# Kernel tuning notes

Hardware: AMD Instinct MI355X
Metric: run time of the kernel (lower is better)

## Reference

```python
import jax, jax.numpy as jnp
import numpy as np

B, N, D, E = 2, 50000, 128, 500000
LN_EPS = 1e-5


def setup_inputs() -> dict:
    key = jax.random.key(0)
    k_h, k_e, k_ws, k_wm = jax.random.split(key, 4)
    scale = 1.0 / np.sqrt(D).astype(np.float32)
    return {
        "h": jax.random.normal(k_h, (B, N, D), dtype=jnp.float32),
        "edge_index": jax.random.randint(k_e, (2, E), 0, N, dtype=jnp.int64),
        "W_self": jax.random.normal(k_ws, (D, D), dtype=jnp.float32) * scale,
        "W_msg": jax.random.normal(k_wm, (D, D), dtype=jnp.float32) * scale,
        "bias": jnp.zeros((D,), dtype=jnp.float32),
        "gamma": jnp.ones((D,), dtype=jnp.float32),
        "beta": jnp.zeros((D,), dtype=jnp.float32),
    }


def reference(h, edge_index, W_self, W_msg, bias, gamma, beta):
    # h: [B,N,D]; edge_index: [2,E] with rows (src, dst).
    n = h.shape[1]
    src, dst = edge_index[0], edge_index[1]

    # Self transform: Linear(dim, dim, bias=False) -> h @ W_self.T
    h_self = jnp.einsum("bnd,od->bno", h, W_self)

    # Gather src node features and transform: msg = W_msg(h[:, src, :])
    msg = jnp.einsum("bed,od->beo", h[:, src, :], W_msg)  # [B,E,D]

    # Scatter-add mean aggregation onto dst nodes.
    h_agg = jax.vmap(lambda m: jax.ops.segment_sum(m, dst, num_segments=n))(msg)  # [B,N,D]
    count = jax.ops.segment_sum(jnp.ones((dst.shape[0],), h.dtype), dst, num_segments=n)
    count = jnp.clip(count, 1.0)[None, :, None]  # clamp(min=1)
    h_agg = h_agg / count

    # Residual + ReLU + (dropout in eval = identity) + LayerNorm
    x = h + jax.nn.relu(h_self + h_agg + bias)
    mu = jnp.mean(x, axis=-1, keepdims=True)
    var = jnp.mean(jnp.square(x - mu), axis=-1, keepdims=True)
    return (x - mu) * jax.lax.rsqrt(var + LN_EPS) * gamma + beta
```

## Files before the change

### kernel.cpp

```cpp
#include <hip/hip_runtime.h>

#define NB 2
#define NN 50000
#define ND 128
#define NE 500000
#define NM (NB * NN)
#define LN_EPS 1e-5f

typedef __attribute__((ext_vector_type(8))) short short8;
typedef __attribute__((ext_vector_type(4))) float f32x4;
typedef __attribute__((ext_vector_type(4))) unsigned short us4;

#define HB_OFF     0
#define AGG_OFF    25600000
#define DEG_OFF    51200000
#define START_OFF  51400000
#define CURSOR_OFF 51600192
#define ELIST_OFF  51800192
#define PART_OFF   53800192
#define WMSG_OFF   53801216

#define SCAN_BLK 512
#define SCAN_NB ((NN + SCAN_BLK - 1) / SCAN_BLK)

__device__ __forceinline__ unsigned short f32_to_bf16(float f) {
    unsigned u = __builtin_bit_cast(unsigned, f);
    unsigned r = u + 0x7FFFu + ((u >> 16) & 1u);
    return (unsigned short)(r >> 16);
}

__device__ __forceinline__ float bf16_to_f32(unsigned short s) {
    unsigned u = ((unsigned)s) << 16;
    return __builtin_bit_cast(float, u);
}

__global__ void count_kernel(const int* __restrict__ ei, int* __restrict__ deg) {
    int e = blockIdx.x * blockDim.x + threadIdx.x;
    if (e < NE) {
        atomicAdd(&deg[ei[NE + e]], 1);
    }
}

__global__ void block_reduce_kernel(const int* __restrict__ deg, int* __restrict__ partials) {
    int i = blockIdx.x * SCAN_BLK + threadIdx.x;
    int v = (i < NN) ? deg[i] : 0;
#pragma unroll
    for (int off = 32; off > 0; off >>= 1) v += __shfl_down(v, off);
    __shared__ int wsum[SCAN_BLK / 64];
    int lane = threadIdx.x & 63;
    int w = threadIdx.x >> 6;
    if (lane == 0) wsum[w] = v;
    __syncthreads();
    if (threadIdx.x == 0) {
        int s = 0;
#pragma unroll
        for (int k = 0; k < SCAN_BLK / 64; ++k) s += wsum[k];
        partials[blockIdx.x] = s;
    }
}

__global__ void partial_scan_kernel(int* __restrict__ partials) {
    __shared__ int tmp[128];
    int t = threadIdx.x;
    int v = (t < SCAN_NB) ? partials[t] : 0;
    tmp[t] = v;
    __syncthreads();
    for (int off = 1; off < 128; off <<= 1) {
        int u = (t >= off) ? tmp[t - off] : 0;
        __syncthreads();
        tmp[t] += u;
        __syncthreads();
    }
    if (t < SCAN_NB) partials[t] = tmp[t] - v;
}

__global__ void block_scan_kernel(const int* __restrict__ deg, const int* __restrict__ partials,
                                  int* __restrict__ start, int* __restrict__ cursor) {
    __shared__ int tmp[SCAN_BLK];
    int t = threadIdx.x;
    int i = blockIdx.x * SCAN_BLK + t;
    int v = (i < NN) ? deg[i] : 0;
    tmp[t] = v;
    __syncthreads();
    for (int off = 1; off < SCAN_BLK; off <<= 1) {
        int u = (t >= off) ? tmp[t - off] : 0;
        __syncthreads();
        tmp[t] += u;
        __syncthreads();
    }
    if (i < NN) {
        int excl = tmp[t] - v + partials[blockIdx.x];
        start[i] = excl;
        cursor[i] = excl;
    }
    if (i == 0) start[NN] = NE;
}

__global__ void fill_kernel(const int* __restrict__ ei, int* __restrict__ cursor,
                            int* __restrict__ elist) {
    int e = blockIdx.x * blockDim.x + threadIdx.x;
    if (e < NE) {
        int d = ei[NE + e];
        int p = atomicAdd(&cursor[d], 1);
        elist[p] = ei[e];
    }
}

__global__ void convert_h_kernel(const float* __restrict__ h, unsigned short* __restrict__ hb16) {
    int i = blockIdx.x * blockDim.x + threadIdx.x;
    if (i >= NM * 16) return;
    int row = i >> 4;
    int c = i & 15;
    const float4 v0 = *(const float4*)(h + (size_t)row * ND + c * 8);
    const float4 v1 = *(const float4*)(h + (size_t)row * ND + c * 8 + 4);
    short8 o;
    o[0] = (short)f32_to_bf16(v0.x); o[1] = (short)f32_to_bf16(v0.y);
    o[2] = (short)f32_to_bf16(v0.z); o[3] = (short)f32_to_bf16(v0.w);
    o[4] = (short)f32_to_bf16(v1.x); o[5] = (short)f32_to_bf16(v1.y);
    o[6] = (short)f32_to_bf16(v1.z); o[7] = (short)f32_to_bf16(v1.w);
    *(short8*)(hb16 + (size_t)row * ND + c * 8) = o;
}

__global__ void convert_wmsg_kernel(const float* __restrict__ Wmsg, unsigned short* __restrict__ wmsg16) {
    int i = blockIdx.x * blockDim.x + threadIdx.x;
    if (i >= 128 * 16) return;
    int row = i >> 4;
    int c = i & 15;
    const float* src = Wmsg + (size_t)row * ND + c * 8;
    short8 o;
#pragma unroll
    for (int j = 0; j < 8; ++j) o[j] = (short)f32_to_bf16(src[j]);
    *(short8*)(wmsg16 + (size_t)row * ND + c * 8) = o;
}

__global__ void agg_kernel(const unsigned short* __restrict__ hb16, const int* __restrict__ start,
                           const int* __restrict__ elist, unsigned short* __restrict__ agg) {
    int wid = (blockIdx.x * blockDim.x + threadIdx.x) >> 6;
    int l = threadIdx.x & 63;
    if (wid >= NM) return;
    int b = wid / NN;
    int n = wid - b * NN;
    int s0 = start[n];
    int d = start[n + 1] - s0;
    const int g = l >> 4;
    const int li = l & 15;
    const unsigned short* hb = hb16 + (size_t)b * NN * ND;
    float s[8] = {0.f, 0.f, 0.f, 0.f, 0.f, 0.f, 0.f, 0.f};
    for (int j0 = 0; j0 < d; j0 += 64) {
        int mye = (j0 + l < d) ? elist[s0 + j0 + l] : -1;
        int cnt = (d - j0 < 64) ? (d - j0) : 64;
        for (int p = 0; p < cnt; p += 4) {
            int e = __shfl(mye, p + g);
            if (p + g < cnt) {
                const short8 v = *(const short8*)(hb + (size_t)e * ND + li * 8);
#pragma unroll
                for (int j = 0; j < 8; ++j) s[j] += bf16_to_f32((unsigned short)v[j]);
            }
        }
    }
#pragma unroll
    for (int j = 0; j < 8; ++j) {
        s[j] += __shfl_xor(s[j], 16);
        s[j] += __shfl_xor(s[j], 32);
    }
    if (g == 0) {
        float sc = 1.0f / (float)(d > 1 ? d : 1);
        short8 o;
#pragma unroll
        for (int j = 0; j < 8; ++j) o[j] = (short)f32_to_bf16(s[j] * sc);
        *(short8*)(agg + (size_t)wid * ND + li * 8) = o;
    }
}

#define GBM 128

__global__ void mfma_agg_kernel(const unsigned short* __restrict__ agg16,
                                const unsigned short* __restrict__ wmsg16,
                                unsigned short* __restrict__ yagg) {
    const int t = threadIdx.x;
    const int w = t >> 6;
    const int l = t & 63;
    const int l15 = l & 15;
    const int lk = l >> 4;
    const int row0 = blockIdx.x * GBM + w * 32;

    f32x4 acc[2][8];
#pragma unroll
    for (int i = 0; i < 2; ++i)
#pragma unroll
        for (int j = 0; j < 8; ++j) acc[i][j] = (f32x4){0.f, 0.f, 0.f, 0.f};

    int rA0 = row0 + l15;      if (rA0 >= NM) rA0 = NM - 1;
    int rA1 = row0 + 16 + l15; if (rA1 >= NM) rA1 = NM - 1;
    const unsigned short* pa0 = agg16 + (size_t)rA0 * ND + lk * 8;
    const unsigned short* pa1 = agg16 + (size_t)rA1 * ND + lk * 8;
    const unsigned short* pb = wmsg16 + (size_t)l15 * ND + lk * 8;

#pragma unroll
    for (int ks = 0; ks < 4; ++ks) {
        const int k0 = ks * 32;
        const short8 a0 = *(const short8*)(pa0 + k0);
        const short8 a1 = *(const short8*)(pa1 + k0);
#pragma unroll
        for (int ct = 0; ct < 8; ++ct) {
            const short8 b = *(const short8*)(pb + ct * 16 * ND + k0);
            acc[0][ct] = __builtin_amdgcn_mfma_f32_16x16x32_bf16(a0, b, acc[0][ct], 0, 0, 0);
            acc[1][ct] = __builtin_amdgcn_mfma_f32_16x16x32_bf16(a1, b, acc[1][ct], 0, 0, 0);
        }
    }

#pragma unroll
    for (int rt = 0; rt < 2; ++rt) {
#pragma unroll
        for (int rg = 0; rg < 4; ++rg) {
            const int row = row0 + rt * 16 + lk * 4 + rg;
            if (row < NM) {
                unsigned short* yrow = yagg + (size_t)row * ND;
#pragma unroll
                for (int ct = 0; ct < 8; ++ct)
                    yrow[ct * 16 + l15] = f32_to_bf16(acc[rt][ct][rg]);
            }
        }
    }
}

#define BM 128
#define BK 16
#define LROW 132

__global__ void fused_gemm_kernel(const float* __restrict__ h, const unsigned short* __restrict__ yagg,
                                  const float* __restrict__ Wself, const float* __restrict__ bias,
                                  const float* __restrict__ gamma, const float* __restrict__ beta,
                                  float* __restrict__ out) {
    __shared__ float As[BK][LROW];
    __shared__ float Bs[BK][LROW];

    const int t = threadIdx.x;
    const int tx = t & 15;
    const int ty = t >> 4;
    const int tx4 = tx * 4;
    const int ty4 = ty * 4;
    const int row0 = blockIdx.x * BM;

    float acc[8][8];
#pragma unroll
    for (int i = 0; i < 8; ++i)
#pragma unroll
        for (int j = 0; j < 8; ++j) acc[i][j] = 0.f;

    for (int kc = 0; kc < 8; ++kc) {
        const int k0 = kc * BK;
        __syncthreads();
#pragma unroll
        for (int s = 0; s < 2; ++s) {
            int f = t + s * 256;
            int r = f >> 2;
            int kk4 = (f & 3) * 4;
            int rg = row0 + r;
            if (rg >= NM) rg = NM - 1;
            const float4 v = *(const float4*)(h + (size_t)rg * ND + k0 + kk4);
            As[kk4 + 0][r] = v.x;
            As[kk4 + 1][r] = v.y;
            As[kk4 + 2][r] = v.z;
            As[kk4 + 3][r] = v.w;
        }
#pragma unroll
        for (int s = 0; s < 2; ++s) {
            int f = t + s * 256;
            int n = f >> 2;
            int kk4 = (f & 3) * 4;
            const float4 v = *(const float4*)(Wself + (size_t)n * ND + k0 + kk4);
            Bs[kk4 + 0][n] = v.x;
            Bs[kk4 + 1][n] = v.y;
            Bs[kk4 + 2][n] = v.z;
            Bs[kk4 + 3][n] = v.w;
        }
        __syncthreads();
#pragma unroll
        for (int kk = 0; kk < BK; ++kk) {
            const float4 a0 = *(const float4*)(&As[kk][ty4]);
            const float4 a1 = *(const float4*)(&As[kk][ty4 + 64]);
            const float4 b0 = *(const float4*)(&Bs[kk][tx4]);
            const float4 b1 = *(const float4*)(&Bs[kk][tx4 + 64]);
            const float a[8] = {a0.x, a0.y, a0.z, a0.w, a1.x, a1.y, a1.z, a1.w};
            const float b[8] = {b0.x, b0.y, b0.z, b0.w, b1.x, b1.y, b1.z, b1.w};
#pragma unroll
            for (int i = 0; i < 8; ++i)
#pragma unroll
                for (int j = 0; j < 8; ++j)
                    acc[i][j] = fmaf(a[i], b[j], acc[i][j]);
        }
    }

    const float4 bi0 = *(const float4*)(bias + tx4);
    const float4 bi1 = *(const float4*)(bias + tx4 + 64);
    const float4 g0 = *(const float4*)(gamma + tx4);
    const float4 g1 = *(const float4*)(gamma + tx4 + 64);
    const float4 be0 = *(const float4*)(beta + tx4);
    const float4 be1 = *(const float4*)(beta + tx4 + 64);
    const float bb[8] = {bi0.x, bi0.y, bi0.z, bi0.w, bi1.x, bi1.y, bi1.z, bi1.w};
    const float gg[8] = {g0.x, g0.y, g0.z, g0.w, g1.x, g1.y, g1.z, g1.w};
    const float ee[8] = {be0.x, be0.y, be0.z, be0.w, be1.x, be1.y, be1.z, be1.w};
    const float inv = 1.0f / (float)ND;

#pragma unroll
    for (int i = 0; i < 8; ++i) {
        const int lm = (i < 4) ? (ty4 + i) : (64 + ty4 + i - 4);
        const int rg = row0 + lm;
        const bool valid = rg < NM;
        const int rc = valid ? rg : NM - 1;
        const float4 h0 = *(const float4*)(h + (size_t)rc * ND + tx4);
        const float4 h1 = *(const float4*)(h + (size_t)rc * ND + tx4 + 64);
        const us4 y0 = *(const us4*)(yagg + (size_t)rc * ND + tx4);
        const us4 y1 = *(const us4*)(yagg + (size_t)rc * ND + tx4 + 64);
        const float hh[8] = {h0.x, h0.y, h0.z, h0.w, h1.x, h1.y, h1.z, h1.w};
        const float yy[8] = {bf16_to_f32(y0[0]), bf16_to_f32(y0[1]), bf16_to_f32(y0[2]), bf16_to_f32(y0[3]),
                             bf16_to_f32(y1[0]), bf16_to_f32(y1[1]), bf16_to_f32(y1[2]), bf16_to_f32(y1[3])};
        float x[8];
        float sum = 0.f, sumsq = 0.f;
#pragma unroll
        for (int j = 0; j < 8; ++j) {
            float y = acc[i][j] + yy[j] + bb[j];
            float xv = hh[j] + (y > 0.f ? y : 0.f);
            x[j] = xv;
            sum += xv;
            sumsq = fmaf(xv, xv, sumsq);
        }
#pragma unroll
        for (int mask = 1; mask < 16; mask <<= 1) {
            sum += __shfl_xor(sum, mask);
            sumsq += __shfl_xor(sumsq, mask);
        }
        const float mu = sum * inv;
        const float var = sumsq * inv - mu * mu;
        const float rstd = rsqrtf(var + LN_EPS);
        if (valid) {
            float4 o0, o1;
            o0.x = (x[0] - mu) * rstd * gg[0] + ee[0];
            o0.y = (x[1] - mu) * rstd * gg[1] + ee[1];
            o0.z = (x[2] - mu) * rstd * gg[2] + ee[2];
            o0.w = (x[3] - mu) * rstd * gg[3] + ee[3];
            o1.x = (x[4] - mu) * rstd * gg[4] + ee[4];
            o1.y = (x[5] - mu) * rstd * gg[5] + ee[5];
            o1.z = (x[6] - mu) * rstd * gg[6] + ee[6];
            o1.w = (x[7] - mu) * rstd * gg[7] + ee[7];
            *(float4*)(out + (size_t)rg * ND + tx4) = o0;
            *(float4*)(out + (size_t)rg * ND + tx4 + 64) = o1;
        }
    }
}

extern "C" void kernel_launch(void* const* d_in, const int* in_sizes, int n_in,
                              void* d_out, int out_size, void* d_ws, size_t ws_size,
                              hipStream_t stream) {
    const float* h = (const float*)d_in[0];
    const int* ei = (const int*)d_in[1];
    const float* Wself = (const float*)d_in[2];
    const float* Wmsg = (const float*)d_in[3];
    const float* bias = (const float*)d_in[4];
    const float* gamma = (const float*)d_in[5];
    const float* beta = (const float*)d_in[6];
    float* out = (float*)d_out;

    char* ws = (char*)d_ws;
    unsigned short* hb16 = (unsigned short*)(ws + HB_OFF);
    unsigned short* yagg = (unsigned short*)(ws + HB_OFF);
    unsigned short* agg16 = (unsigned short*)(ws + AGG_OFF);
    unsigned short* wmsg16 = (unsigned short*)(ws + WMSG_OFF);
    int* deg = (int*)(ws + DEG_OFF);
    int* start = (int*)(ws + START_OFF);
    int* cursor = (int*)(ws + CURSOR_OFF);
    int* elist = (int*)(ws + ELIST_OFF);
    int* partials = (int*)(ws + PART_OFF);

    hipMemsetAsync(deg, 0, NN * sizeof(int), stream);

    count_kernel<<<(NE + 255) / 256, 256, 0, stream>>>(ei, deg);
    block_reduce_kernel<<<SCAN_NB, SCAN_BLK, 0, stream>>>(deg, partials);
    partial_scan_kernel<<<1, 128, 0, stream>>>(partials);
    block_scan_kernel<<<SCAN_NB, SCAN_BLK, 0, stream>>>(deg, partials, start, cursor);
    fill_kernel<<<(NE + 255) / 256, 256, 0, stream>>>(ei, cursor, elist);

    convert_h_kernel<<<(NM * 16 + 255) / 256, 256, 0, stream>>>(h, hb16);
    convert_wmsg_kernel<<<(128 * 16 + 255) / 256, 256, 0, stream>>>(Wmsg, wmsg16);

    agg_kernel<<<(NM * 64 + 255) / 256, 256, 0, stream>>>(hb16, start, elist, agg16);

    int nblocks = (NM + GBM - 1) / GBM;
    mfma_agg_kernel<<<nblocks, 256, 0, stream>>>(agg16, wmsg16, yagg);

    fused_gemm_kernel<<<nblocks, 256, 0, stream>>>(h, yagg, Wself, bias, gamma, beta, out);
}
```

Baseline: 209.2 us.

## Fuse MFMA message GEMM into self-GEMM epilogue kernel and merge prep kernels

```diff
diff --git a/kernel.cpp b/kernel.cpp
--- a/kernel.cpp
+++ b/kernel.cpp
@@ -9,7 +9,6 @@
 
 typedef __attribute__((ext_vector_type(8))) short short8;
 typedef __attribute__((ext_vector_type(4))) float f32x4;
-typedef __attribute__((ext_vector_type(4))) unsigned short us4;
 
 #define HB_OFF     0
 #define AGG_OFF    25600000
@@ -23,6 +22,10 @@
 #define SCAN_BLK 512
 #define SCAN_NB ((NN + SCAN_BLK - 1) / SCAN_BLK)
 
+#define CONVH_NB ((NM * 16 + 255) / 256)
+#define CONVW_NB 8
+#define COUNT_NB ((NE + 255) / 256)
+
 __device__ __forceinline__ unsigned short f32_to_bf16(float f) {
     unsigned u = __builtin_bit_cast(unsigned, f);
     unsigned r = u + 0x7FFFu + ((u >> 16) & 1u);
@@ -34,10 +37,35 @@
     return __builtin_bit_cast(float, u);
 }
 
-__global__ void count_kernel(const int* __restrict__ ei, int* __restrict__ deg) {
-    int e = blockIdx.x * blockDim.x + threadIdx.x;
-    if (e < NE) {
-        atomicAdd(&deg[ei[NE + e]], 1);
+__global__ void prep_kernel(const float* __restrict__ h, unsigned short* __restrict__ hb16,
+                            const float* __restrict__ Wmsg, unsigned short* __restrict__ wmsg16,
+                            const int* __restrict__ ei, int* __restrict__ deg) {
+    const int bid = blockIdx.x;
+    if (bid < CONVH_NB) {
+        int i = bid * 256 + threadIdx.x;
+        if (i >= NM * 16) return;
+        int row = i >> 4;
+        int c = i & 15;
+        const float4 v0 = *(const float4*)(h + (size_t)row * ND + c * 8);
+        const float4 v1 = *(const float4*)(h + (size_t)row * ND + c * 8 + 4);
+        short8 o;
+        o[0] = (short)f32_to_bf16(v0.x); o[1] = (short)f32_to_bf16(v0.y);
+        o[2] = (short)f32_to_bf16(v0.z); o[3] = (short)f32_to_bf16(v0.w);
+        o[4] = (short)f32_to_bf16(v1.x); o[5] = (short)f32_to_bf16(v1.y);
+        o[6] = (short)f32_to_bf16(v1.z); o[7] = (short)f32_to_bf16(v1.w);
+        *(short8*)(hb16 + (size_t)row * ND + c * 8) = o;
+    } else if (bid < CONVH_NB + CONVW_NB) {
+        int i = (bid - CONVH_NB) * 256 + threadIdx.x;
+        int row = i >> 4;
+        int c = i & 15;
+        const float* src = Wmsg + (size_t)row * ND + c * 8;
+        short8 o;
+#pragma unroll
+        for (int j = 0; j < 8; ++j) o[j] = (short)f32_to_bf16(src[j]);
+        *(short8*)(wmsg16 + (size_t)row * ND + c * 8) = o;
+    } else {
+        int e = (bid - CONVH_NB - CONVW_NB) * 256 + threadIdx.x;
+        if (e < NE) atomicAdd(&deg[ei[NE + e]], 1);
     }
 }
 
@@ -104,33 +132,6 @@
         int p = atomicAdd(&cursor[d], 1);
         elist[p] = ei[e];
     }
-}
-
-__global__ void convert_h_kernel(const float* __restrict__ h, unsigned short* __restrict__ hb16) {
-    int i = blockIdx.x * blockDim.x + threadIdx.x;
-    if (i >= NM * 16) return;
-    int row = i >> 4;
-    int c = i & 15;
-    const float4 v0 = *(const float4*)(h + (size_t)row * ND + c * 8);
-    const float4 v1 = *(const float4*)(h + (size_t)row * ND + c * 8 + 4);
-    short8 o;
-    o[0] = (short)f32_to_bf16(v0.x); o[1] = (short)f32_to_bf16(v0.y);
-    o[2] = (short)f32_to_bf16(v0.z); o[3] = (short)f32_to_bf16(v0.w);
-    o[4] = (short)f32_to_bf16(v1.x); o[5] = (short)f32_to_bf16(v1.y);
-    o[6] = (short)f32_to_bf16(v1.z); o[7] = (short)f32_to_bf16(v1.w);
-    *(short8*)(hb16 + (size_t)row * ND + c * 8) = o;
-}
-
-__global__ void convert_wmsg_kernel(const float* __restrict__ Wmsg, unsigned short* __restrict__ wmsg16) {
-    int i = blockIdx.x * blockDim.x + threadIdx.x;
-    if (i >= 128 * 16) return;
-    int row = i >> 4;
-    int c = i & 15;
-    const float* src = Wmsg + (size_t)row * ND + c * 8;
-    short8 o;
-#pragma unroll
-    for (int j = 0; j < 8; ++j) o[j] = (short)f32_to_bf16(src[j]);
-    *(short8*)(wmsg16 + (size_t)row * ND + c * 8) = o;
 }
 
 __global__ void agg_kernel(const unsigned short* __restrict__ hb16, const int* __restrict__ start,
@@ -149,7 +150,18 @@
     for (int j0 = 0; j0 < d; j0 += 64) {
         int mye = (j0 + l < d) ? elist[s0 + j0 + l] : -1;
         int cnt = (d - j0 < 64) ? (d - j0) : 64;
-        for (int p = 0; p < cnt; p += 4) {
+        int p = 0;
+        for (; p + 8 <= cnt; p += 8) {
+            int e0 = __shfl(mye, p + g);
+            int e1 = __shfl(mye, p + 4 + g);
+            const short8 v0 = *(const short8*)(hb + (size_t)e0 * ND + li * 8);
+            const short8 v1 = *(const short8*)(hb + (size_t)e1 * ND + li * 8);
+#pragma unroll
+            for (int j = 0; j < 8; ++j) s[j] += bf16_to_f32((unsigned short)v0[j]);
+#pragma unroll
+            for (int j = 0; j < 8; ++j) s[j] += bf16_to_f32((unsigned short)v1[j]);
+        }
+        for (; p < cnt; p += 4) {
             int e = __shfl(mye, p + g);
             if (p + g < cnt) {
                 const short8 v = *(const short8*)(hb + (size_t)e * ND + li * 8);
@@ -172,29 +184,40 @@
     }
 }
 
-#define GBM 128
-
-__global__ void mfma_agg_kernel(const unsigned short* __restrict__ agg16,
-                                const unsigned short* __restrict__ wmsg16,
-                                unsigned short* __restrict__ yagg) {
+#define BM 128
+#define BK 32
+#define LROW 132
+
+__global__ void fused_gemm_kernel(const float* __restrict__ h,
+                                  const unsigned short* __restrict__ agg16,
+                                  const unsigned short* __restrict__ wmsg16,
+                                  const float* __restrict__ Wself,
+                                  const float* __restrict__ bias,
+                                  const float* __restrict__ gamma,
+                                  const float* __restrict__ beta,
+                                  float* __restrict__ out) {
+    __shared__ float As[BK][LROW];
+    __shared__ float Bs[BK][LROW];
+
     const int t = threadIdx.x;
     const int w = t >> 6;
     const int l = t & 63;
     const int l15 = l & 15;
     const int lk = l >> 4;
-    const int row0 = blockIdx.x * GBM + w * 32;
-
-    f32x4 acc[2][8];
+    const int row0 = blockIdx.x * BM;
+    const int wbase = w * 32;
+
+    f32x4 macc[2][8];
 #pragma unroll
     for (int i = 0; i < 2; ++i)
 #pragma unroll
-        for (int j = 0; j < 8; ++j) acc[i][j] = (f32x4){0.f, 0.f, 0.f, 0.f};
-
-    int rA0 = row0 + l15;      if (rA0 >= NM) rA0 = NM - 1;
-    int rA1 = row0 + 16 + l15; if (rA1 >= NM) rA1 = NM - 1;
+        for (int j = 0; j < 8; ++j) macc[i][j] = (f32x4){0.f, 0.f, 0.f, 0.f};
+
+    int rA0 = row0 + wbase + l15;      if (rA0 >= NM) rA0 = NM - 1;
+    int rA1 = row0 + wbase + 16 + l15; if (rA1 >= NM) rA1 = NM - 1;
     const unsigned short* pa0 = agg16 + (size_t)rA0 * ND + lk * 8;
     const unsigned short* pa1 = agg16 + (size_t)rA1 * ND + lk * 8;
-    const unsigned short* pb = wmsg16 + (size_t)l15 * ND + lk * 8;
+    const unsigned short* pb  = wmsg16 + (size_t)l15 * ND + lk * 8;
 
 #pragma unroll
     for (int ks = 0; ks < 4; ++ks) {
@@ -204,43 +227,10 @@
 #pragma unroll
         for (int ct = 0; ct < 8; ++ct) {
             const short8 b = *(const short8*)(pb + ct * 16 * ND + k0);
-            acc[0][ct] = __builtin_amdgcn_mfma_f32_16x16x32_bf16(a0, b, acc[0][ct], 0, 0, 0);
-            acc[1][ct] = __builtin_amdgcn_mfma_f32_16x16x32_bf16(a1, b, acc[1][ct], 0, 0, 0);
-        }
-    }
-
-#pragma unroll
-    for (int rt = 0; rt < 2; ++rt) {
-#pragma unroll
-        for (int rg = 0; rg < 4; ++rg) {
-            const int row = row0 + rt * 16 + lk * 4 + rg;
-            if (row < NM) {
-                unsigned short* yrow = yagg + (size_t)row * ND;
-#pragma unroll
-                for (int ct = 0; ct < 8; ++ct)
-                    yrow[ct * 16 + l15] = f32_to_bf16(acc[rt][ct][rg]);
-            }
-        }
-    }
-}
-
-#define BM 128
-#define BK 16
-#define LROW 132
-
-__global__ void fused_gemm_kernel(const float* __restrict__ h, const unsigned short* __restrict__ yagg,
-                                  const float* __restrict__ Wself, const float* __restrict__ bias,
-                                  const float* __restrict__ gamma, const float* __restrict__ beta,
-                                  float* __restrict__ out) {
-    __shared__ float As[BK][LROW];
-    __shared__ float Bs[BK][LROW];
-
-    const int t = threadIdx.x;
-    const int tx = t & 15;
-    const int ty = t >> 4;
-    const int tx4 = tx * 4;
-    const int ty4 = ty * 4;
-    const int row0 = blockIdx.x * BM;
+            macc[0][ct] = __builtin_amdgcn_mfma_f32_16x16x32_bf16(a0, b, macc[0][ct], 0, 0, 0);
+            macc[1][ct] = __builtin_amdgcn_mfma_f32_16x16x32_bf16(a1, b, macc[1][ct], 0, 0, 0);
+        }
+    }
 
     float acc[8][8];
 #pragma unroll
@@ -248,14 +238,14 @@
 #pragma unroll
         for (int j = 0; j < 8; ++j) acc[i][j] = 0.f;
 
-    for (int kc = 0; kc < 8; ++kc) {
+    for (int kc = 0; kc < 4; ++kc) {
         const int k0 = kc * BK;
         __syncthreads();
 #pragma unroll
-        for (int s = 0; s < 2; ++s) {
+        for (int s = 0; s < 4; ++s) {
             int f = t + s * 256;
-            int r = f >> 2;
-            int kk4 = (f & 3) * 4;
+            int r = f >> 3;
+            int kk4 = (f & 7) * 4;
             int rg = row0 + r;
             if (rg >= NM) rg = NM - 1;
             const float4 v = *(const float4*)(h + (size_t)rg * ND + k0 + kk4);
@@ -265,10 +255,10 @@
             As[kk4 + 3][r] = v.w;
         }
 #pragma unroll
-        for (int s = 0; s < 2; ++s) {
+        for (int s = 0; s < 4; ++s) {
             int f = t + s * 256;
-            int n = f >> 2;
-            int kk4 = (f & 3) * 4;
+            int n = f >> 3;
+            int kk4 = (f & 7) * 4;
             const float4 v = *(const float4*)(Wself + (size_t)n * ND + k0 + kk4);
             Bs[kk4 + 0][n] = v.x;
             Bs[kk4 + 1][n] = v.y;
@@ -278,74 +268,59 @@
         __syncthreads();
 #pragma unroll
         for (int kk = 0; kk < BK; ++kk) {
-            const float4 a0 = *(const float4*)(&As[kk][ty4]);
-            const float4 a1 = *(const float4*)(&As[kk][ty4 + 64]);
-            const float4 b0 = *(const float4*)(&Bs[kk][tx4]);
-            const float4 b1 = *(const float4*)(&Bs[kk][tx4 + 64]);
-            const float a[8] = {a0.x, a0.y, a0.z, a0.w, a1.x, a1.y, a1.z, a1.w};
-            const float b[8] = {b0.x, b0.y, b0.z, b0.w, b1.x, b1.y, b1.z, b1.w};
+            const float4 a0 = *(const float4*)(&As[kk][wbase + lk * 4]);
+            const float4 a1 = *(const float4*)(&As[kk][wbase + 16 + lk * 4]);
+            float bv[8];
+#pragma unroll
+            for (int ct = 0; ct < 8; ++ct) bv[ct] = Bs[kk][ct * 16 + l15];
+            const float av[8] = {a0.x, a0.y, a0.z, a0.w, a1.x, a1.y, a1.z, a1.w};
 #pragma unroll
             for (int i = 0; i < 8; ++i)
 #pragma unroll
                 for (int j = 0; j < 8; ++j)
-                    acc[i][j] = fmaf(a[i], b[j], acc[i][j]);
-        }
-    }
-
-    const float4 bi0 = *(const float4*)(bias + tx4);
-    const float4 bi1 = *(const float4*)(bias + tx4 + 64);
-    const float4 g0 = *(const float4*)(gamma + tx4);
-    const float4 g1 = *(const float4*)(gamma + tx4 + 64);
-    const float4 be0 = *(const float4*)(beta + tx4);
-    const float4 be1 = *(const float4*)(beta + tx4 + 64);
-    const float bb[8] = {bi0.x, bi0.y, bi0.z, bi0.w, bi1.x, bi1.y, bi1.z, bi1.w};
-    const float gg[8] = {g0.x, g0.y, g0.z, g0.w, g1.x, g1.y, g1.z, g1.w};
-    const float ee[8] = {be0.x, be0.y, be0.z, be0.w, be1.x, be1.y, be1.z, be1.w};
+                    acc[i][j] = fmaf(av[i], bv[j], acc[i][j]);
+        }
+    }
+
+    float bb[8], gg[8], ee[8];
+#pragma unroll
+    for (int ct = 0; ct < 8; ++ct) {
+        bb[ct] = bias[ct * 16 + l15];
+        gg[ct] = gamma[ct * 16 + l15];
+        ee[ct] = beta[ct * 16 + l15];
+    }
     const float inv = 1.0f / (float)ND;
-
-#pragma unroll
-    for (int i = 0; i < 8; ++i) {
-        const int lm = (i < 4) ? (ty4 + i) : (64 + ty4 + i - 4);
-        const int rg = row0 + lm;
-        const bool valid = rg < NM;
-        const int rc = valid ? rg : NM - 1;
-        const float4 h0 = *(const float4*)(h + (size_t)rc * ND + tx4);
-        const float4 h1 = *(const float4*)(h + (size_t)rc * ND + tx4 + 64);
-        const us4 y0 = *(const us4*)(yagg + (size_t)rc * ND + tx4);
-        const us4 y1 = *(const us4*)(yagg + (size_t)rc * ND + tx4 + 64);
-        const float hh[8] = {h0.x, h0.y, h0.z, h0.w, h1.x, h1.y, h1.z, h1.w};
-        const float yy[8] = {bf16_to_f32(y0[0]), bf16_to_f32(y0[1]), bf16_to_f32(y0[2]), bf16_to_f32(y0[3]),
-                             bf16_to_f32(y1[0]), bf16_to_f32(y1[1]), bf16_to_f32(y1[2]), bf16_to_f32(y1[3])};
-        float x[8];
-        float sum = 0.f, sumsq = 0.f;
-#pragma unroll
-        for (int j = 0; j < 8; ++j) {
-            float y = acc[i][j] + yy[j] + bb[j];
-            float xv = hh[j] + (y > 0.f ? y : 0.f);
-            x[j] = xv;
-            sum += xv;
-            sumsq = fmaf(xv, xv, sumsq);
-        }
-#pragma unroll
-        for (int mask = 1; mask < 16; mask <<= 1) {
-            sum += __shfl_xor(sum, mask);
-            sumsq += __shfl_xor(sumsq, mask);
-        }
-        const float mu = sum * inv;
-        const float var = sumsq * inv - mu * mu;
-        const float rstd = rsqrtf(var + LN_EPS);
-        if (valid) {
-            float4 o0, o1;
-            o0.x = (x[0] - mu) * rstd * gg[0] + ee[0];
-            o0.y = (x[1] - mu) * rstd * gg[1] + ee[1];
-            o0.z = (x[2] - mu) * rstd * gg[2] + ee[2];
-            o0.w = (x[3] - mu) * rstd * gg[3] + ee[3];
-            o1.x = (x[4] - mu) * rstd * gg[4] + ee[4];
-            o1.y = (x[5] - mu) * rstd * gg[5] + ee[5];
-            o1.z = (x[6] - mu) * rstd * gg[6] + ee[6];
-            o1.w = (x[7] - mu) * rstd * gg[7] + ee[7];
-            *(float4*)(out + (size_t)rg * ND + tx4) = o0;
-            *(float4*)(out + (size_t)rg * ND + tx4 + 64) = o1;
+#pragma unroll
+    for (int rt = 0; rt < 2; ++rt) {
+#pragma unroll
+        for (int rg = 0; rg < 4; ++rg) {
+            const int row = row0 + wbase + rt * 16 + lk * 4 + rg;
+            const bool valid = row < NM;
+            const int rc = valid ? row : NM - 1;
+            const float* hrow = h + (size_t)rc * ND;
+            float x[8];
+            float sum = 0.f, sq = 0.f;
+#pragma unroll
+            for (int ct = 0; ct < 8; ++ct) {
+                float y = acc[rt * 4 + rg][ct] + macc[rt][ct][rg] + bb[ct];
+                float xv = hrow[ct * 16 + l15] + (y > 0.f ? y : 0.f);
+                x[ct] = xv;
+                sum += xv;
+                sq = fmaf(xv, xv, sq);
+            }
+#pragma unroll
+            for (int m = 1; m < 16; m <<= 1) {
+                sum += __shfl_xor(sum, m);
+                sq += __shfl_xor(sq, m);
+            }
+            const float mu = sum * inv;
+            const float rstd = rsqrtf(sq * inv - mu * mu + LN_EPS);
+            if (valid) {
+                float* orow = out + (size_t)row * ND;
+#pragma unroll
+                for (int ct = 0; ct < 8; ++ct)
+                    orow[ct * 16 + l15] = (x[ct] - mu) * rstd * gg[ct] + ee[ct];
+            }
         }
     }
 }
@@ -364,7 +339,6 @@
 
     char* ws = (char*)d_ws;
     unsigned short* hb16 = (unsigned short*)(ws + HB_OFF);
-    unsigned short* yagg = (unsigned short*)(ws + HB_OFF);
     unsigned short* agg16 = (unsigned short*)(ws + AGG_OFF);
     unsigned short* wmsg16 = (unsigned short*)(ws + WMSG_OFF);
     int* deg = (int*)(ws + DEG_OFF);
@@ -375,19 +349,14 @@
 
     hipMemsetAsync(deg, 0, NN * sizeof(int), stream);
 
-    count_kernel<<<(NE + 255) / 256, 256, 0, stream>>>(ei, deg);
+    prep_kernel<<<CONVH_NB + CONVW_NB + COUNT_NB, 256, 0, stream>>>(h, hb16, Wmsg, wmsg16, ei, deg);
     block_reduce_kernel<<<SCAN_NB, SCAN_BLK, 0, stream>>>(deg, partials);
     partial_scan_kernel<<<1, 128, 0, stream>>>(partials);
     block_scan_kernel<<<SCAN_NB, SCAN_BLK, 0, stream>>>(deg, partials, start, cursor);
     fill_kernel<<<(NE + 255) / 256, 256, 0, stream>>>(ei, cursor, elist);
 
-    convert_h_kernel<<<(NM * 16 + 255) / 256, 256, 0, stream>>>(h, hb16);
-    convert_wmsg_kernel<<<(128 * 16 + 255) / 256, 256, 0, stream>>>(Wmsg, wmsg16);
-
     agg_kernel<<<(NM * 64 + 255) / 256, 256, 0, stream>>>(hb16, start, elist, agg16);
 
-    int nblocks = (NM + GBM - 1) / GBM;
-    mfma_agg_kernel<<<nblocks, 256, 0, stream>>>(agg16, wmsg16, yagg);
-
-    fused_gemm_kernel<<<nblocks, 256, 0, stream>>>(h, yagg, Wself, bias, gamma, beta, out);
-}
+    int nblocks = (NM + BM - 1) / BM;
+    fused_gemm_kernel<<<nblocks, 256, 0, stream>>>(h, agg16, wmsg16, Wself, bias, gamma, beta, out);
+}
```

Result: no change. 213.3 us (+2.0%).
